# Optimization experiments

Measured on AMD Instinct MI355X. Metric: run time of the kernel, lower is better.

## Reference

```python
import jax, jax.numpy as jnp
import numpy as np

IN_FEATURES = 2048
HIDDEN_FEATURES = 8192  # = num_experts * expert_hidden
TOKENS = 16384


def setup_inputs() -> dict:
    key = jax.random.key(0)
    k1, k2, k3, k4 = jax.random.split(key, 4)
    scale = 1.0 / np.sqrt(IN_FEATURES)
    x = jax.random.normal(k1, (TOKENS, IN_FEATURES), dtype=jnp.float32)
    w1 = jax.random.normal(k2, (HIDDEN_FEATURES, IN_FEATURES), dtype=jnp.float32) * scale
    w2 = jax.random.normal(k3, (HIDDEN_FEATURES, IN_FEATURES), dtype=jnp.float32) * scale
    w3 = jax.random.normal(k4, (HIDDEN_FEATURES, IN_FEATURES), dtype=jnp.float32) * scale
    return {"x": x, "w1": w1, "w2": w2, "w3": w3, "num_experts": 8}


def reference(x, w1, w2, w3, num_experts):
    # Block-sparse MoE SwiGLU FFN. Tokens are sorted by expert and balanced:
    # token block e uses hidden slice e of w1/w2/w3 (the stk topology).
    tokens, d = x.shape
    hidden = w1.shape[0]
    e = num_experts
    h_e = hidden // e            # per-expert hidden size
    t_e = tokens // e            # tokens per expert
    xe = x.reshape(e, t_e, d)                  # [E, Te, D]
    w1e = w1.reshape(e, h_e, d)                # [E, He, D]
    w2e = w2.reshape(e, h_e, d)
    w3e = w3.reshape(e, h_e, d)
    # sdd: sparse output of x @ w^T restricted to each token's expert block
    h1 = jnp.einsum("etd,ehd->eth", xe, w1e)   # [E, Te, He]
    h2 = jnp.einsum("etd,ehd->eth", xe, w2e)
    g = jax.nn.silu(h1) * h2                   # fused SiLU gating
    # dsd: block-sparse @ dense w3 -> dense [tokens, D]
    out = jnp.einsum("eth,ehd->etd", g, w3e)
    return out.reshape(tokens, d)
```

## Files before the change

### kernel.cpp

```cpp
#include <hip/hip_runtime.h>
#include <stdint.h>


#define NEXP   8
#define TOKENS 16384
#define D_IN   2048
#define HIDDEN 8192
#define T_E    2048
#define H_E    1024

typedef __attribute__((ext_vector_type(8))) __bf16 bf16x8;
typedef __attribute__((ext_vector_type(4))) float  f32x4;

__device__ __forceinline__ void async_ld16(const void* g, void* l) {
  __builtin_amdgcn_global_load_lds(
      (const __attribute__((address_space(1))) void*)g,
      (__attribute__((address_space(3))) void*)l, 16, 0, 0);
}

__device__ __forceinline__ unsigned short f2bf(float f) {
  union { float f; uint32_t u; } c; c.f = f;
  uint32_t u = c.u;
  u += 0x7FFFu + ((u >> 16) & 1u);
  return (unsigned short)(u >> 16);
}

__device__ __forceinline__ void tile_map(int s, int& mt, int& nt) {
  int g = s >> 2, w = s & 3;
  mt = (g & 3) * 2 + (w & 1);
  nt = (g >> 2) * 2 + (w >> 1);
}

__global__ __launch_bounds__(256) void cvt_kernel(
    const float* __restrict__ in, unsigned short* __restrict__ out, int n4) {
  int i = blockIdx.x * 256 + threadIdx.x;
  if (i >= n4) return;
  float4 v = ((const float4*)in)[i];
  ushort4 r;
  r.x = f2bf(v.x); r.y = f2bf(v.y); r.z = f2bf(v.z); r.w = f2bf(v.w);
  ((ushort4*)out)[i] = r;
}

__global__ __launch_bounds__(256) void transpose_w3_kernel(
    const float* __restrict__ w3, unsigned short* __restrict__ w3t) {
  __shared__ unsigned short tile[32][33];
  const int d0 = blockIdx.x * 32;
  const int h0 = blockIdx.y * 32;
  const int tx = threadIdx.x;
  const int ty = threadIdx.y;
#pragma unroll
  for (int j = 0; j < 32; j += 8)
    tile[ty + j][tx] = f2bf(w3[(size_t)(h0 + ty + j) * D_IN + d0 + tx]);
  __syncthreads();
  const int e   = h0 >> 10;
  const int hl0 = h0 & 1023;
#pragma unroll
  for (int j = 0; j < 32; j += 8)
    w3t[((size_t)e * D_IN + d0 + ty + j) * H_E + hl0 + tx] = tile[tx][ty + j];
}

__global__ __launch_bounds__(512, 2) void gemm1_kernel(
    const unsigned short* __restrict__ xb,
    const unsigned short* __restrict__ w1b,
    const unsigned short* __restrict__ w2b,
    unsigned short* __restrict__ g)
{
  extern __shared__ char lds[];
  char* const AsB  = lds;
  char* const B1sB = lds + 65536;
  char* const B2sB = lds + 98304;

  const int bid = blockIdx.x;
  const int e   = bid & 7;
  int mt, nt; tile_map(bid >> 3, mt, nt);
  const int m0 = mt * 256;
  const int n0 = nt * 128;

  const unsigned short* A  = xb  + (size_t)e * T_E * D_IN + (size_t)m0 * D_IN;
  const unsigned short* B1 = w1b + (size_t)e * H_E * D_IN + (size_t)n0 * D_IN;
  const unsigned short* B2 = w2b + (size_t)e * H_E * D_IN + (size_t)n0 * D_IN;

  const int tid  = threadIdx.x;
  const int wave = tid >> 6;
  const int lane = tid & 63;
  const int wm   = wave >> 2;
  const int wn   = wave & 3;
  const int lm   = lane & 15;
  const int qs   = lane >> 4;

  const int srow   = tid >> 2;
  const int schunk = tid & 3;
  const int sc     = (schunk ^ ((srow >> 1) & 3)) * 8;
  const unsigned short* aS0 = A  + (size_t)srow * D_IN + sc;
  const unsigned short* aS1 = A  + (size_t)(128 + srow) * D_IN + sc;
  const unsigned short* b1S = B1 + (size_t)srow * D_IN + sc;
  const unsigned short* b2S = B2 + (size_t)srow * D_IN + sc;
  char* const ldsA0 = AsB  + tid * 16;
  char* const ldsA1 = AsB  + 8192 + tid * 16;
  char* const ldsB1 = B1sB + tid * 16;
  char* const ldsB2 = B2sB + tid * 16;

  int offA[8], offB[2];
#pragma unroll
  for (int mi = 0; mi < 8; ++mi) {
    int r = wm * 128 + mi * 16 + lm;
    offA[mi] = r * 64 + ((qs ^ ((r >> 1) & 3)) * 16);
  }
#pragma unroll
  for (int ni = 0; ni < 2; ++ni) {
    int r = wn * 32 + ni * 16 + lm;
    offB[ni] = r * 64 + ((qs ^ ((r >> 1) & 3)) * 16);
  }

  f32x4 acc1[8][2], acc2[8][2];
#pragma unroll
  for (int mi = 0; mi < 8; ++mi)
#pragma unroll
    for (int ni = 0; ni < 2; ++ni) {
      acc1[mi][ni] = (f32x4){0.f, 0.f, 0.f, 0.f};
      acc2[mi][ni] = (f32x4){0.f, 0.f, 0.f, 0.f};
    }

#define G1_STAGE(t)                                          \
  { const int sl_ = (t) & 3;                                 \
    async_ld16(aS0 + (t) * 32, ldsA0 + sl_ * 16384);         \
    async_ld16(aS1 + (t) * 32, ldsA1 + sl_ * 16384);         \
    async_ld16(b1S + (t) * 32, ldsB1 + sl_ * 8192);          \
    async_ld16(b2S + (t) * 32, ldsB2 + sl_ * 8192); }

  G1_STAGE(0); G1_STAGE(1); G1_STAGE(2);

  const int NT = D_IN / 32;
  for (int t = 0; t < NT; ++t) {
    if (t < NT - 2)       asm volatile("s_waitcnt vmcnt(8)" ::: "memory");
    else if (t == NT - 2) asm volatile("s_waitcnt vmcnt(4)" ::: "memory");
    else                  asm volatile("s_waitcnt vmcnt(0)" ::: "memory");
    __builtin_amdgcn_s_barrier();
    __builtin_amdgcn_sched_barrier(0);
    if (t + 3 < NT) { G1_STAGE(t + 3); }

    const char* At  = AsB  + (t & 3) * 16384;
    const char* B1t = B1sB + (t & 3) * 8192;
    const char* B2t = B2sB + (t & 3) * 8192;
    bf16x8 af[8], b1f[2], b2f[2];
#pragma unroll
    for (int ni = 0; ni < 2; ++ni) {
      b1f[ni] = *(const bf16x8*)(B1t + offB[ni]);
      b2f[ni] = *(const bf16x8*)(B2t + offB[ni]);
    }
#pragma unroll
    for (int mi = 0; mi < 8; ++mi)
      af[mi] = *(const bf16x8*)(At + offA[mi]);

    __builtin_amdgcn_s_setprio(1);
#pragma unroll
    for (int mi = 0; mi < 8; ++mi)
#pragma unroll
      for (int ni = 0; ni < 2; ++ni) {
        acc1[mi][ni] = __builtin_amdgcn_mfma_f32_16x16x32_bf16(
            af[mi], b1f[ni], acc1[mi][ni], 0, 0, 0);
        acc2[mi][ni] = __builtin_amdgcn_mfma_f32_16x16x32_bf16(
            af[mi], b2f[ni], acc2[mi][ni], 0, 0, 0);
      }
    __builtin_amdgcn_s_setprio(0);
    asm volatile("s_waitcnt lgkmcnt(0)" ::: "memory");
    __builtin_amdgcn_sched_barrier(0);
  }
#undef G1_STAGE

  unsigned short* grow = g + (size_t)e * T_E * H_E;
  const int q4 = qs * 4;
#pragma unroll
  for (int mi = 0; mi < 8; ++mi) {
    const int row = m0 + wm * 128 + mi * 16 + q4;
#pragma unroll
    for (int ni = 0; ni < 2; ++ni) {
      const int col = n0 + wn * 32 + ni * 16 + lm;
#pragma unroll
      for (int r = 0; r < 4; ++r) {
        float v1 = acc1[mi][ni][r];
        float v2 = acc2[mi][ni][r];
        float gv = (v1 / (1.0f + __expf(-v1))) * v2;
        grow[(size_t)(row + r) * H_E + col] = f2bf(gv);
      }
    }
  }
}

__global__ __launch_bounds__(512, 2) void gemm2_kernel(
    const unsigned short* __restrict__ g,
    const unsigned short* __restrict__ w3t,
    float* __restrict__ out)
{
  extern __shared__ char lds[];
  char* const AsB = lds;
  char* const BsB = lds + 65536;

  const int bid = blockIdx.x;
  const int e   = bid & 7;
  int mt, nt; tile_map(bid >> 3, mt, nt);
  const int m0 = mt * 256;
  const int n0 = nt * 256;

  const unsigned short* A = g   + (size_t)e * T_E * H_E  + (size_t)m0 * H_E;
  const unsigned short* B = w3t + (size_t)e * D_IN * H_E + (size_t)n0 * H_E;

  const int tid  = threadIdx.x;
  const int wave = tid >> 6;
  const int lane = tid & 63;
  const int wm   = wave >> 2;
  const int wn   = wave & 3;
  const int lm   = lane & 15;
  const int qs   = lane >> 4;

  const int srow   = tid >> 2;
  const int schunk = tid & 3;
  const int sc     = (schunk ^ ((srow >> 1) & 3)) * 8;
  const unsigned short* aS0 = A + (size_t)srow * H_E + sc;
  const unsigned short* aS1 = A + (size_t)(128 + srow) * H_E + sc;
  const unsigned short* bS0 = B + (size_t)srow * H_E + sc;
  const unsigned short* bS1 = B + (size_t)(128 + srow) * H_E + sc;
  char* const ldsA0 = AsB + tid * 16;
  char* const ldsA1 = AsB + 8192 + tid * 16;
  char* const ldsB0 = BsB + tid * 16;
  char* const ldsB1 = BsB + 8192 + tid * 16;

  int offA[8], offB[4];
#pragma unroll
  for (int mi = 0; mi < 8; ++mi) {
    int r = wm * 128 + mi * 16 + lm;
    offA[mi] = r * 64 + ((qs ^ ((r >> 1) & 3)) * 16);
  }
#pragma unroll
  for (int ni = 0; ni < 4; ++ni) {
    int r = wn * 64 + ni * 16 + lm;
    offB[ni] = r * 64 + ((qs ^ ((r >> 1) & 3)) * 16);
  }

  f32x4 acc[8][4];
#pragma unroll
  for (int mi = 0; mi < 8; ++mi)
#pragma unroll
    for (int ni = 0; ni < 4; ++ni) acc[mi][ni] = (f32x4){0.f, 0.f, 0.f, 0.f};

#define G2_STAGE(t)                                          \
  { const int sl_ = (t) & 3;                                 \
    async_ld16(aS0 + (t) * 32, ldsA0 + sl_ * 16384);         \
    async_ld16(aS1 + (t) * 32, ldsA1 + sl_ * 16384);         \
    async_ld16(bS0 + (t) * 32, ldsB0 + sl_ * 16384);         \
    async_ld16(bS1 + (t) * 32, ldsB1 + sl_ * 16384); }

  G2_STAGE(0); G2_STAGE(1); G2_STAGE(2);

  const int NT = H_E / 32;
  for (int t = 0; t < NT; ++t) {
    if (t < NT - 2)       asm volatile("s_waitcnt vmcnt(8)" ::: "memory");
    else if (t == NT - 2) asm volatile("s_waitcnt vmcnt(4)" ::: "memory");
    else                  asm volatile("s_waitcnt vmcnt(0)" ::: "memory");
    __builtin_amdgcn_s_barrier();
    __builtin_amdgcn_sched_barrier(0);
    if (t + 3 < NT) { G2_STAGE(t + 3); }

    const char* At = AsB + (t & 3) * 16384;
    const char* Bt = BsB + (t & 3) * 16384;
    bf16x8 af[8], bfr[4];
#pragma unroll
    for (int ni = 0; ni < 4; ++ni)
      bfr[ni] = *(const bf16x8*)(Bt + offB[ni]);
#pragma unroll
    for (int mi = 0; mi < 8; ++mi)
      af[mi] = *(const bf16x8*)(At + offA[mi]);

    __builtin_amdgcn_s_setprio(1);
#pragma unroll
    for (int mi = 0; mi < 8; ++mi)
#pragma unroll
      for (int ni = 0; ni < 4; ++ni)
        acc[mi][ni] = __builtin_amdgcn_mfma_f32_16x16x32_bf16(
            af[mi], bfr[ni], acc[mi][ni], 0, 0, 0);
    __builtin_amdgcn_s_setprio(0);
    asm volatile("s_waitcnt lgkmcnt(0)" ::: "memory");
    __builtin_amdgcn_sched_barrier(0);
  }
#undef G2_STAGE

  float* orow = out + (size_t)e * T_E * D_IN;
  const int q4 = qs * 4;
#pragma unroll
  for (int mi = 0; mi < 8; ++mi) {
    const int row = m0 + wm * 128 + mi * 16 + q4;
#pragma unroll
    for (int ni = 0; ni < 4; ++ni) {
      const int col = n0 + wn * 64 + ni * 16 + lm;
#pragma unroll
      for (int r = 0; r < 4; ++r)
        orow[(size_t)(row + r) * D_IN + col] = acc[mi][ni][r];
    }
  }
}

extern "C" void kernel_launch(void* const* d_in, const int* in_sizes, int n_in,
                              void* d_out, int out_size, void* d_ws, size_t ws_size,
                              hipStream_t stream) {
  const float* x  = (const float*)d_in[0];
  const float* w1 = (const float*)d_in[1];
  const float* w2 = (const float*)d_in[2];
  const float* w3 = (const float*)d_in[3];
  float* out = (float*)d_out;

  static bool attr_done = false;
  if (!attr_done) {
    hipFuncSetAttribute(reinterpret_cast<const void*>(gemm1_kernel),
                        hipFuncAttributeMaxDynamicSharedMemorySize, 131072);
    hipFuncSetAttribute(reinterpret_cast<const void*>(gemm2_kernel),
                        hipFuncAttributeMaxDynamicSharedMemorySize, 131072);
    attr_done = true;
  }

  char* ws = (char*)d_ws;
  unsigned short* xb  = (unsigned short*)(ws);
  unsigned short* w1b = (unsigned short*)(ws + 67108864);
  unsigned short* w2b = (unsigned short*)(ws + 100663296);
  unsigned short* w3t = (unsigned short*)(ws + 134217728);
  unsigned short* gbuf= (unsigned short*)(ws + 167772160);

  cvt_kernel<<<(TOKENS * D_IN / 4 + 255) / 256, 256, 0, stream>>>(x, xb, TOKENS * D_IN / 4);
  cvt_kernel<<<(HIDDEN * D_IN / 4 + 255) / 256, 256, 0, stream>>>(w1, w1b, HIDDEN * D_IN / 4);
  cvt_kernel<<<(HIDDEN * D_IN / 4 + 255) / 256, 256, 0, stream>>>(w2, w2b, HIDDEN * D_IN / 4);

  transpose_w3_kernel<<<dim3(D_IN / 32, HIDDEN / 32), dim3(32, 8), 0, stream>>>(w3, w3t);

  gemm1_kernel<<<NEXP * 64, 512, 131072, stream>>>(xb, w1b, w2b, gbuf);

  gemm2_kernel<<<NEXP * 64, 512, 131072, stream>>>(gbuf, w3t, out);
}
```

Before: 564.0 us.

## Split GEMM main loops into two halves interleaving async loads with MFMA; merge convert kernels

In both GEMM kernels, each k-step is split into two halves. The prefetch global-to-LDS loads for the next-next-next stage are issued in two parts between the halves, so global load issue interleaves with MFMA work and fewer A fragments stay live at once. The three fp32-to-bf16 conversion launches are also merged into one kernel to cut launch overhead. The waitcnt counts stay the same, so correctness depends on the vmcnt ordering still matching the split issue order.

```diff
diff --git a/kernel.cpp b/kernel.cpp
--- a/kernel.cpp
+++ b/kernel.cpp
@@ -31,14 +31,22 @@
   nt = (g >> 2) * 2 + (w >> 1);
 }
 
-__global__ __launch_bounds__(256) void cvt_kernel(
-    const float* __restrict__ in, unsigned short* __restrict__ out, int n4) {
+#define X4 (TOKENS * D_IN / 4)
+#define W4 (HIDDEN * D_IN / 4)
+__global__ __launch_bounds__(256) void cvt3_kernel(
+    const float* __restrict__ x,  const float* __restrict__ w1,
+    const float* __restrict__ w2,
+    unsigned short* __restrict__ xb, unsigned short* __restrict__ w1b,
+    unsigned short* __restrict__ w2b) {
   int i = blockIdx.x * 256 + threadIdx.x;
-  if (i >= n4) return;
-  float4 v = ((const float4*)in)[i];
+  const float* in; unsigned short* out; int j;
+  if (i < X4)            { in = x;  out = xb;  j = i; }
+  else if (i < X4 + W4)  { in = w1; out = w1b; j = i - X4; }
+  else                   { in = w2; out = w2b; j = i - X4 - W4; }
+  float4 v = ((const float4*)in)[j];
   ushort4 r;
   r.x = f2bf(v.x); r.y = f2bf(v.y); r.z = f2bf(v.z); r.w = f2bf(v.w);
-  ((ushort4*)out)[i] = r;
+  ((ushort4*)out)[j] = r;
 }
 
 __global__ __launch_bounds__(256) void transpose_w3_kernel(
@@ -137,30 +145,58 @@
     else                  asm volatile("s_waitcnt vmcnt(0)" ::: "memory");
     __builtin_amdgcn_s_barrier();
     __builtin_amdgcn_sched_barrier(0);
-    if (t + 3 < NT) { G1_STAGE(t + 3); }
 
     const char* At  = AsB  + (t & 3) * 16384;
     const char* B1t = B1sB + (t & 3) * 8192;
     const char* B2t = B2sB + (t & 3) * 8192;
-    bf16x8 af[8], b1f[2], b2f[2];
+
+    if (t + 3 < NT) {
+      const int sl_ = (t + 3) & 3;
+      async_ld16(aS0 + (t + 3) * 32, ldsA0 + sl_ * 16384);
+      async_ld16(b1S + (t + 3) * 32, ldsB1 + sl_ * 8192);
+    }
+    bf16x8 b1f[2], b2f[2], afA[4];
 #pragma unroll
     for (int ni = 0; ni < 2; ++ni) {
       b1f[ni] = *(const bf16x8*)(B1t + offB[ni]);
       b2f[ni] = *(const bf16x8*)(B2t + offB[ni]);
     }
 #pragma unroll
-    for (int mi = 0; mi < 8; ++mi)
-      af[mi] = *(const bf16x8*)(At + offA[mi]);
+    for (int mi = 0; mi < 4; ++mi)
+      afA[mi] = *(const bf16x8*)(At + offA[mi]);
 
     __builtin_amdgcn_s_setprio(1);
 #pragma unroll
-    for (int mi = 0; mi < 8; ++mi)
+    for (int mi = 0; mi < 4; ++mi)
 #pragma unroll
       for (int ni = 0; ni < 2; ++ni) {
         acc1[mi][ni] = __builtin_amdgcn_mfma_f32_16x16x32_bf16(
-            af[mi], b1f[ni], acc1[mi][ni], 0, 0, 0);
+            afA[mi], b1f[ni], acc1[mi][ni], 0, 0, 0);
         acc2[mi][ni] = __builtin_amdgcn_mfma_f32_16x16x32_bf16(
-            af[mi], b2f[ni], acc2[mi][ni], 0, 0, 0);
+            afA[mi], b2f[ni], acc2[mi][ni], 0, 0, 0);
+      }
+    __builtin_amdgcn_s_setprio(0);
+    __builtin_amdgcn_sched_barrier(0);
+
+    if (t + 3 < NT) {
+      const int sl_ = (t + 3) & 3;
+      async_ld16(aS1 + (t + 3) * 32, ldsA1 + sl_ * 16384);
+      async_ld16(b2S + (t + 3) * 32, ldsB2 + sl_ * 8192);
+    }
+    bf16x8 afB[4];
+#pragma unroll
+    for (int mi = 0; mi < 4; ++mi)
+      afB[mi] = *(const bf16x8*)(At + offA[mi + 4]);
+
+    __builtin_amdgcn_s_setprio(1);
+#pragma unroll
+    for (int mi = 0; mi < 4; ++mi)
+#pragma unroll
+      for (int ni = 0; ni < 2; ++ni) {
+        acc1[mi + 4][ni] = __builtin_amdgcn_mfma_f32_16x16x32_bf16(
+            afB[mi], b1f[ni], acc1[mi + 4][ni], 0, 0, 0);
+        acc2[mi + 4][ni] = __builtin_amdgcn_mfma_f32_16x16x32_bf16(
+            afB[mi], b2f[ni], acc2[mi + 4][ni], 0, 0, 0);
       }
     __builtin_amdgcn_s_setprio(0);
     asm volatile("s_waitcnt lgkmcnt(0)" ::: "memory");
@@ -259,25 +295,50 @@
     else                  asm volatile("s_waitcnt vmcnt(0)" ::: "memory");
     __builtin_amdgcn_s_barrier();
     __builtin_amdgcn_sched_barrier(0);
-    if (t + 3 < NT) { G2_STAGE(t + 3); }
 
     const char* At = AsB + (t & 3) * 16384;
     const char* Bt = BsB + (t & 3) * 16384;
-    bf16x8 af[8], bfr[4];
+
+    if (t + 3 < NT) {
+      const int sl_ = (t + 3) & 3;
+      async_ld16(aS0 + (t + 3) * 32, ldsA0 + sl_ * 16384);
+      async_ld16(bS0 + (t + 3) * 32, ldsB0 + sl_ * 16384);
+    }
+    bf16x8 bfr[4], afA[4];
 #pragma unroll
     for (int ni = 0; ni < 4; ++ni)
       bfr[ni] = *(const bf16x8*)(Bt + offB[ni]);
 #pragma unroll
-    for (int mi = 0; mi < 8; ++mi)
-      af[mi] = *(const bf16x8*)(At + offA[mi]);
+    for (int mi = 0; mi < 4; ++mi)
+      afA[mi] = *(const bf16x8*)(At + offA[mi]);
 
     __builtin_amdgcn_s_setprio(1);
 #pragma unroll
-    for (int mi = 0; mi < 8; ++mi)
+    for (int mi = 0; mi < 4; ++mi)
 #pragma unroll
       for (int ni = 0; ni < 4; ++ni)
         acc[mi][ni] = __builtin_amdgcn_mfma_f32_16x16x32_bf16(
-            af[mi], bfr[ni], acc[mi][ni], 0, 0, 0);
+            afA[mi], bfr[ni], acc[mi][ni], 0, 0, 0);
+    __builtin_amdgcn_s_setprio(0);
+    __builtin_amdgcn_sched_barrier(0);
+
+    if (t + 3 < NT) {
+      const int sl_ = (t + 3) & 3;
+      async_ld16(aS1 + (t + 3) * 32, ldsA1 + sl_ * 16384);
+      async_ld16(bS1 + (t + 3) * 32, ldsB1 + sl_ * 16384);
+    }
+    bf16x8 afB[4];
+#pragma unroll
+    for (int mi = 0; mi < 4; ++mi)
+      afB[mi] = *(const bf16x8*)(At + offA[mi + 4]);
+
+    __builtin_amdgcn_s_setprio(1);
+#pragma unroll
+    for (int mi = 0; mi < 4; ++mi)
+#pragma unroll
+      for (int ni = 0; ni < 4; ++ni)
+        acc[mi + 4][ni] = __builtin_amdgcn_mfma_f32_16x16x32_bf16(
+            afB[mi], bfr[ni], acc[mi + 4][ni], 0, 0, 0);
     __builtin_amdgcn_s_setprio(0);
     asm volatile("s_waitcnt lgkmcnt(0)" ::: "memory");
     __builtin_amdgcn_sched_barrier(0);
@@ -324,9 +385,7 @@
   unsigned short* w3t = (unsigned short*)(ws + 134217728);
   unsigned short* gbuf= (unsigned short*)(ws + 167772160);
 
-  cvt_kernel<<<(TOKENS * D_IN / 4 + 255) / 256, 256, 0, stream>>>(x, xb, TOKENS * D_IN / 4);
-  cvt_kernel<<<(HIDDEN * D_IN / 4 + 255) / 256, 256, 0, stream>>>(w1, w1b, HIDDEN * D_IN / 4);
-  cvt_kernel<<<(HIDDEN * D_IN / 4 + 255) / 256, 256, 0, stream>>>(w2, w2b, HIDDEN * D_IN / 4);
+  cvt3_kernel<<<(X4 + 2 * W4) / 256, 256, 0, stream>>>(x, w1, w2, xb, w1b, w2b);
 
   transpose_w3_kernel<<<dim3(D_IN / 32, HIDDEN / 32), dim3(32, 8), 0, stream>>>(w3, w3t);
 
```

Result: no change. 557.3 us (-1.2%).
